# Kernel optimization log

Hardware: AMD Instinct MI355X
Metric: run time of the kernel (lower is better)

Reference implementation:

```python
import jax, jax.numpy as jnp
import numpy as np

C = 16        # C1 = C2 = Cout
LMAX = 2
# Sparse path set for Lmax=2, max_rank_other=1, allow_epsilon=False, k_policy='k0'.
# Enumeration order (L1 outer, L2 inner) matches the torch module's weight layout.
PATHS = [(0, 0), (0, 1), (0, 2), (1, 0), (1, 1), (2, 0)]  # Lout = L1 + L2, k_delta=0
# Fused einsums: contract channels a,b with per-path weight W[o,a,b];
# output tensor indices ordered as (free i's of A) then (free j's of B), per _einsum_for_path.
EQS = {
    (0, 0): 'na,nb,oab->no',
    (0, 1): 'na,nbi,oab->noi',
    (0, 2): 'na,nbij,oab->noij',
    (1, 0): 'nai,nb,oab->noi',
    (1, 1): 'nai,nbj,oab->noij',
    (2, 0): 'naij,nb,oab->noij',
}


def split_by_rank_o3(x, channels):
    """Split flat O(3)-graded features into {(s, L): block} with block shape (N, C, 3^L...)."""
    blocks = {}
    idx = 0
    n = x.shape[0]
    for s in (0, 1):
        for L in range(LMAX + 1):
            d = channels * 3 ** L
            blocks[(s, L)] = x[:, idx:idx + d].reshape((n, channels) + (3,) * L)
            idx += d
    return blocks


def _forward(x1, x2, weight):
    n = x1.shape[0]
    A = split_by_rank_o3(x1, C)
    B = split_by_rank_o3(x2, C)
    # assume_pseudo_zero & no epsilon: only s=0 blocks are used; s_out is always 0.
    out = {L: jnp.zeros((n, C) + (3,) * L, dtype=x1.dtype) for L in range(LMAX + 1)}
    w_idx = 0
    blk = C * C * C
    for (L1, L2) in PATHS:
        Wp = weight[w_idx:w_idx + blk].reshape(C, C, C)  # (Cout, C1, C2)
        w_idx += blk
        Lout = L1 + L2
        out[Lout] = out[Lout] + jnp.einsum(EQS[(L1, L2)], A[(0, L1)], B[(0, L2)], Wp)
    # merge_by_rank_o3: s=0 blocks (L=0..Lmax) then s=1 blocks (all zero here)
    parts = [out[L].reshape(n, -1) for L in range(LMAX + 1)]
    parts += [jnp.zeros((n, C * 3 ** L), dtype=x1.dtype) for L in range(LMAX + 1)]
    return jnp.concatenate(parts, axis=-1)  # (N, 2*C*13) = (N, 416)


def setup_inputs() -> dict:
    key = jax.random.key(0)
    k1, k2, k3 = jax.random.split(key, 3)
    N = 200000
    dim = 2 * C * (1 + 3 + 9)  # 416
    x1 = jax.random.normal(k1, (N, dim), dtype=jnp.float32)
    x2 = jax.random.normal(k2, (N, dim), dtype=jnp.float32)
    weight = jax.random.normal(k3, (len(PATHS) * C * C * C,), dtype=jnp.float32) * 0.02
    return {"x1": x1, "x2": x2, "weight": weight}


def reference(x1, x2, weight):
    return _forward(x1, x2, weight)
```

## Files before the change

kernel.cpp:

```cpp
#include <hip/hip_runtime.h>


constexpr int TILE_R  = 16;
constexpr int NTHR    = 256;
constexpr int WSTRIDE = 260;
constexpr int WSLICE  = 16 * WSTRIDE;
constexpr int RSTRIDE = 212;

__device__ __forceinline__ float dot16(const float* __restrict__ w, const float* a) {
    float s0 = 0.f, s1 = 0.f, s2 = 0.f, s3 = 0.f;
#pragma unroll
    for (int k = 0; k < 4; ++k) {
        float4 v = *(const float4*)(w + 4 * k);
        s0 = fmaf(v.x, a[4 * k + 0], s0);
        s1 = fmaf(v.y, a[4 * k + 1], s1);
        s2 = fmaf(v.z, a[4 * k + 2], s2);
        s3 = fmaf(v.w, a[4 * k + 3], s3);
    }
    return (s0 + s1) + (s2 + s3);
}

__device__ __forceinline__ void accum_t(const float* __restrict__ w,
                                        const float* a0, float* t) {
#pragma unroll
    for (int a = 0; a < 16; ++a) {
        float av = a0[a];
        const float* wr = w + 16 * a;
#pragma unroll
        for (int k = 0; k < 4; ++k) {
            float4 v = *(const float4*)(wr + 4 * k);
            t[4*k+0] = fmaf(v.x, av, t[4*k+0]);
            t[4*k+1] = fmaf(v.y, av, t[4*k+1]);
            t[4*k+2] = fmaf(v.z, av, t[4*k+2]);
            t[4*k+3] = fmaf(v.w, av, t[4*k+3]);
        }
    }
}

__device__ __forceinline__ void load_w2(const float* __restrict__ wgt, float* ws,
                                        int p0, int p1, int tid) {
#pragma unroll
    for (int s = tid; s < 2048; s += NTHR) {
        int m   = s >> 10;
        int rem = s & 1023;
        int oo  = rem >> 6;
        int off = (rem & 63) << 2;
        float4 v = *(const float4*)(wgt + (m ? p1 : p0) * 4096 + (rem << 2));
        *(float4*)&ws[m * WSLICE + oo * WSTRIDE + off] = v;
    }
}

__global__ __launch_bounds__(NTHR, 2)
void tp_kernel(const float* __restrict__ x1, const float* __restrict__ x2,
               const float* __restrict__ wgt, float* __restrict__ out, int N)
{
    __shared__ float Ws[2 * WSLICE];
    __shared__ float As[TILE_R * RSTRIDE];
    __shared__ float Bs[TILE_R * RSTRIDE];

    const int tid  = threadIdx.x;
    const int wave = tid >> 6;
    const int lane = tid & 63;
    const int o    = (wave << 2) + (lane >> 4);
    const int r    = lane & 15;
    const long long row0 = (long long)blockIdx.x * TILE_R;

    for (int idx = tid; idx < TILE_R * 52; idx += NTHR) {
        int rr = idx / 52, cc = idx - rr * 52;
        float4 va = make_float4(0.f, 0.f, 0.f, 0.f), vb = va;
        if (row0 + rr < N) {
            long long g = (row0 + rr) * 416 + cc * 4;
            va = *(const float4*)(x1 + g);
            vb = *(const float4*)(x2 + g);
        }
        *(float4*)&As[rr * RSTRIDE + cc * 4] = va;
        *(float4*)&Bs[rr * RSTRIDE + cc * 4] = vb;
    }
    load_w2(wgt, Ws, 0, 1, tid);
    __syncthreads();

    float a0[16], b0[16], b1[48];
#pragma unroll
    for (int k = 0; k < 4; ++k) {
        float4 v = *(const float4*)&As[r * RSTRIDE + 4 * k];
        a0[4*k+0] = v.x; a0[4*k+1] = v.y; a0[4*k+2] = v.z; a0[4*k+3] = v.w;
        float4 u = *(const float4*)&Bs[r * RSTRIDE + 4 * k];
        b0[4*k+0] = u.x; b0[4*k+1] = u.y; b0[4*k+2] = u.z; b0[4*k+3] = u.w;
    }
#pragma unroll
    for (int k = 0; k < 12; ++k) {
        float4 v = *(const float4*)&Bs[r * RSTRIDE + 16 + 4 * k];
        b1[4*k+0] = v.x; b1[4*k+1] = v.y; b1[4*k+2] = v.z; b1[4*k+3] = v.w;
    }

    float o0 = 0.f, o1[3] = {0.f, 0.f, 0.f};
    float o2[9] = {0.f,0.f,0.f,0.f,0.f,0.f,0.f,0.f,0.f};

    {
        const float* w0 = &Ws[o * WSTRIDE];
#pragma unroll
        for (int a = 0; a < 16; ++a)
            o0 = fmaf(a0[a], dot16(w0 + 16 * a, b0), o0);

        const float* w1 = &Ws[WSLICE + o * WSTRIDE];
        float t[16] = {0.f,0.f,0.f,0.f,0.f,0.f,0.f,0.f,0.f,0.f,0.f,0.f,0.f,0.f,0.f,0.f};
        accum_t(w1, a0, t);
#pragma unroll
        for (int b = 0; b < 16; ++b) {
            o1[0] = fmaf(t[b], b1[3*b+0], o1[0]);
            o1[1] = fmaf(t[b], b1[3*b+1], o1[1]);
            o1[2] = fmaf(t[b], b1[3*b+2], o1[2]);
        }
    }
    __syncthreads();
    load_w2(wgt, Ws, 2, 3, tid);
    __syncthreads();

    {
        const float* w2 = &Ws[o * WSTRIDE];
        float t[16] = {0.f,0.f,0.f,0.f,0.f,0.f,0.f,0.f,0.f,0.f,0.f,0.f,0.f,0.f,0.f,0.f};
        accum_t(w2, a0, t);
#pragma unroll
        for (int b = 0; b < 16; ++b) {
            const float* b2 = &Bs[r * RSTRIDE + 64 + 9 * b];
#pragma unroll
            for (int k = 0; k < 9; ++k) o2[k] = fmaf(t[b], b2[k], o2[k]);
        }

        const float* w3 = &Ws[WSLICE + o * WSTRIDE];
#pragma unroll
        for (int a = 0; a < 16; ++a) {
            float u = dot16(w3 + 16 * a, b0);
            const float* a1 = &As[r * RSTRIDE + 16 + 3 * a];
            o1[0] = fmaf(u, a1[0], o1[0]);
            o1[1] = fmaf(u, a1[1], o1[1]);
            o1[2] = fmaf(u, a1[2], o1[2]);
        }
    }
    __syncthreads();
    load_w2(wgt, Ws, 4, 5, tid);
    __syncthreads();

    {
        const float* w4 = &Ws[o * WSTRIDE];
#pragma unroll
        for (int a = 0; a < 16; ++a) {
            const float* wa = w4 + 16 * a;
            float v0 = 0.f, v1 = 0.f, v2 = 0.f;
#pragma unroll
            for (int k = 0; k < 4; ++k) {
                float4 w = *(const float4*)(wa + 4 * k);
                v0 = fmaf(w.x, b1[12*k+0], v0); v1 = fmaf(w.x, b1[12*k+ 1], v1); v2 = fmaf(w.x, b1[12*k+ 2], v2);
                v0 = fmaf(w.y, b1[12*k+3], v0); v1 = fmaf(w.y, b1[12*k+ 4], v1); v2 = fmaf(w.y, b1[12*k+ 5], v2);
                v0 = fmaf(w.z, b1[12*k+6], v0); v1 = fmaf(w.z, b1[12*k+ 7], v1); v2 = fmaf(w.z, b1[12*k+ 8], v2);
                v0 = fmaf(w.w, b1[12*k+9], v0); v1 = fmaf(w.w, b1[12*k+10], v1); v2 = fmaf(w.w, b1[12*k+11], v2);
            }
            const float* a1 = &As[r * RSTRIDE + 16 + 3 * a];
            float a10 = a1[0], a11 = a1[1], a12 = a1[2];
            o2[0] = fmaf(a10, v0, o2[0]); o2[1] = fmaf(a10, v1, o2[1]); o2[2] = fmaf(a10, v2, o2[2]);
            o2[3] = fmaf(a11, v0, o2[3]); o2[4] = fmaf(a11, v1, o2[4]); o2[5] = fmaf(a11, v2, o2[5]);
            o2[6] = fmaf(a12, v0, o2[6]); o2[7] = fmaf(a12, v1, o2[7]); o2[8] = fmaf(a12, v2, o2[8]);
        }

        const float* w5 = &Ws[WSLICE + o * WSTRIDE];
#pragma unroll
        for (int a = 0; a < 16; ++a) {
            float u = dot16(w5 + 16 * a, b0);
            const float* a2 = &As[r * RSTRIDE + 64 + 9 * a];
#pragma unroll
            for (int k = 0; k < 9; ++k) o2[k] = fmaf(u, a2[k], o2[k]);
        }
    }

    __syncthreads();
    {
        float* dst = &As[r * RSTRIDE];
        dst[o] = o0;
        dst[16 + 3*o + 0] = o1[0];
        dst[16 + 3*o + 1] = o1[1];
        dst[16 + 3*o + 2] = o1[2];
#pragma unroll
        for (int k = 0; k < 9; ++k) dst[64 + 9*o + k] = o2[k];
    }
    __syncthreads();
    for (int idx = tid; idx < TILE_R * 104; idx += NTHR) {
        int rr = idx / 104, cc = idx - rr * 104;
        if (row0 + rr < N) {
            float4 v = make_float4(0.f, 0.f, 0.f, 0.f);
            if (cc < 52) v = *(const float4*)&As[rr * RSTRIDE + (cc << 2)];
            *(float4*)&out[(row0 + rr) * 416 + (cc << 2)] = v;
        }
    }
}

extern "C" void kernel_launch(void* const* d_in, const int* in_sizes, int n_in,
                              void* d_out, int out_size, void* d_ws, size_t ws_size,
                              hipStream_t stream) {
    const float* x1  = (const float*)d_in[0];
    const float* x2  = (const float*)d_in[1];
    const float* wgt = (const float*)d_in[2];
    float* out = (float*)d_out;
    const int N = in_sizes[0] / 416;
    const int grid = (N + TILE_R - 1) / TILE_R;
    hipLaunchKernelGGL(tp_kernel, dim3(grid), dim3(NTHR), 0, stream, x1, x2, wgt, out, N);
}
```

Measured before the change: 988.4 us.

## Read weights from global via wave-uniform scalar loads and transpose activation tiles in LDS

The weight tiles are no longer staged in shared memory. Each wave now owns one output channel, selected with readfirstlane, so its weight reads are wave-uniform and can be served by scalar or cache loads straight from global memory. The block grows to 1024 threads and 64 rows, and the rank-1 and rank-2 activation blocks are stored transposed in LDS so each Cartesian component's 16 channels are contiguous for float4 reads. This removes the per-stage weight reload and its barriers, at the cost of larger blocks, lower occupancy flexibility and heavier register use.

```diff
diff --git a/kernel.cpp b/kernel.cpp
--- a/kernel.cpp
+++ b/kernel.cpp
@@ -1,11 +1,10 @@
 #include <hip/hip_runtime.h>
 
 
-constexpr int TILE_R  = 16;
-constexpr int NTHR    = 256;
-constexpr int WSTRIDE = 260;
-constexpr int WSLICE  = 16 * WSTRIDE;
-constexpr int RSTRIDE = 212;
+constexpr int NTHR   = 1024;
+constexpr int TILE_R = 64;
+constexpr int ASTR   = 228;
+constexpr int BSTR   = 212;
 
 __device__ __forceinline__ float dot16(const float* __restrict__ w, const float* a) {
     float s0 = 0.f, s1 = 0.f, s2 = 0.f, s3 = 0.f;
@@ -37,158 +36,153 @@
     }
 }
 
-__device__ __forceinline__ void load_w2(const float* __restrict__ wgt, float* ws,
-                                        int p0, int p1, int tid) {
-#pragma unroll
-    for (int s = tid; s < 2048; s += NTHR) {
-        int m   = s >> 10;
-        int rem = s & 1023;
-        int oo  = rem >> 6;
-        int off = (rem & 63) << 2;
-        float4 v = *(const float4*)(wgt + (m ? p1 : p0) * 4096 + (rem << 2));
-        *(float4*)&ws[m * WSLICE + oo * WSTRIDE + off] = v;
-    }
-}
-
-__global__ __launch_bounds__(NTHR, 2)
+__device__ __forceinline__ void ld16(const float* p, float* d) {
+#pragma unroll
+    for (int k = 0; k < 4; ++k) {
+        float4 v = *(const float4*)(p + 4 * k);
+        d[4*k+0] = v.x; d[4*k+1] = v.y; d[4*k+2] = v.z; d[4*k+3] = v.w;
+    }
+}
+
+__global__ __launch_bounds__(NTHR)
 void tp_kernel(const float* __restrict__ x1, const float* __restrict__ x2,
                const float* __restrict__ wgt, float* __restrict__ out, int N)
 {
-    __shared__ float Ws[2 * WSLICE];
-    __shared__ float As[TILE_R * RSTRIDE];
-    __shared__ float Bs[TILE_R * RSTRIDE];
-
-    const int tid  = threadIdx.x;
-    const int wave = tid >> 6;
-    const int lane = tid & 63;
-    const int o    = (wave << 2) + (lane >> 4);
-    const int r    = lane & 15;
+    __shared__ __align__(16) float As[TILE_R * ASTR];
+    __shared__ __align__(16) float Bs[TILE_R * BSTR];
+
+    const int tid = threadIdx.x;
     const long long row0 = (long long)blockIdx.x * TILE_R;
 
     for (int idx = tid; idx < TILE_R * 52; idx += NTHR) {
-        int rr = idx / 52, cc = idx - rr * 52;
+        int rr = idx / 52, c4 = idx - rr * 52;
         float4 va = make_float4(0.f, 0.f, 0.f, 0.f), vb = va;
         if (row0 + rr < N) {
-            long long g = (row0 + rr) * 416 + cc * 4;
+            long long g = (row0 + rr) * 416 + c4 * 4;
             va = *(const float4*)(x1 + g);
             vb = *(const float4*)(x2 + g);
         }
-        *(float4*)&As[rr * RSTRIDE + cc * 4] = va;
-        *(float4*)&Bs[rr * RSTRIDE + cc * 4] = vb;
-    }
-    load_w2(wgt, Ws, 0, 1, tid);
+        if (c4 < 4) {
+            *(float4*)&As[rr * ASTR + 4 * c4] = va;
+            *(float4*)&Bs[rr * BSTR + 4 * c4] = vb;
+        } else {
+            float fa[4] = {va.x, va.y, va.z, va.w};
+            float fb[4] = {vb.x, vb.y, vb.z, vb.w};
+#pragma unroll
+            for (int q = 0; q < 4; ++q) {
+                int c = 4 * c4 + q;
+                int da, db;
+                if (c < 64) {
+                    int n = c - 16;
+                    int a = (n * 21846) >> 16;
+                    int i = n - 3 * a;
+                    da = 16 + 4 * a + i;
+                    db = 16 + 16 * i + a;
+                } else {
+                    int n = c - 64;
+                    int a = (n * 7282) >> 16;
+                    int k = n - 9 * a;
+                    da = 80 + 16 * k + a;
+                    db = 64 + 16 * k + a;
+                }
+                As[rr * ASTR + da] = fa[q];
+                Bs[rr * BSTR + db] = fb[q];
+            }
+        }
+    }
     __syncthreads();
 
-    float a0[16], b0[16], b1[48];
-#pragma unroll
-    for (int k = 0; k < 4; ++k) {
-        float4 v = *(const float4*)&As[r * RSTRIDE + 4 * k];
-        a0[4*k+0] = v.x; a0[4*k+1] = v.y; a0[4*k+2] = v.z; a0[4*k+3] = v.w;
-        float4 u = *(const float4*)&Bs[r * RSTRIDE + 4 * k];
-        b0[4*k+0] = u.x; b0[4*k+1] = u.y; b0[4*k+2] = u.z; b0[4*k+3] = u.w;
-    }
-#pragma unroll
-    for (int k = 0; k < 12; ++k) {
-        float4 v = *(const float4*)&Bs[r * RSTRIDE + 16 + 4 * k];
-        b1[4*k+0] = v.x; b1[4*k+1] = v.y; b1[4*k+2] = v.z; b1[4*k+3] = v.w;
-    }
-
-    float o0 = 0.f, o1[3] = {0.f, 0.f, 0.f};
+    const int o = __builtin_amdgcn_readfirstlane((int)(threadIdx.x >> 6));
+    const int r = tid & 63;
+    const float* __restrict__ wp = wgt + o * 256;
+    const float* Ar = &As[r * ASTR];
+    const float* Br = &Bs[r * BSTR];
+
+    float a0[16], b0[16];
+    ld16(Ar, a0);
+    ld16(Br, b0);
+
+    float o0 = 0.f;
+    float o1[3] = {0.f, 0.f, 0.f};
     float o2[9] = {0.f,0.f,0.f,0.f,0.f,0.f,0.f,0.f,0.f};
 
+#pragma unroll
+    for (int a = 0; a < 16; ++a)
+        o0 = fmaf(a0[a], dot16(wp + 16 * a, b0), o0);
+
+    float t1[16], t2[16];
+#pragma unroll
+    for (int k = 0; k < 16; ++k) { t1[k] = 0.f; t2[k] = 0.f; }
+    accum_t(wp + 4096, a0, t1);
+    accum_t(wp + 8192, a0, t2);
+
+#pragma unroll
+    for (int j = 0; j < 3; ++j) {
+        float br[16];
+        ld16(Br + 16 + 16 * j, br);
+#pragma unroll
+        for (int b = 0; b < 16; ++b)
+            o1[j] = fmaf(t1[b], br[b], o1[j]);
+#pragma unroll
+        for (int a = 0; a < 16; ++a) {
+            float v = dot16(wp + 16384 + 16 * a, br);
+            float4 a1 = *(const float4*)(Ar + 16 + 4 * a);
+            o2[0 + j] = fmaf(a1.x, v, o2[0 + j]);
+            o2[3 + j] = fmaf(a1.y, v, o2[3 + j]);
+            o2[6 + j] = fmaf(a1.z, v, o2[6 + j]);
+        }
+    }
+
+#pragma unroll
+    for (int k = 0; k < 9; ++k) {
+        float br[16];
+        ld16(Br + 64 + 16 * k, br);
+#pragma unroll
+        for (int b = 0; b < 16; ++b)
+            o2[k] = fmaf(t2[b], br[b], o2[k]);
+    }
+
+#pragma unroll
+    for (int a = 0; a < 16; ++a) {
+        float u = dot16(wp + 12288 + 16 * a, b0);
+        float4 a1 = *(const float4*)(Ar + 16 + 4 * a);
+        o1[0] = fmaf(u, a1.x, o1[0]);
+        o1[1] = fmaf(u, a1.y, o1[1]);
+        o1[2] = fmaf(u, a1.z, o1[2]);
+    }
+
     {
-        const float* w0 = &Ws[o * WSTRIDE];
+        float u[16];
 #pragma unroll
         for (int a = 0; a < 16; ++a)
-            o0 = fmaf(a0[a], dot16(w0 + 16 * a, b0), o0);
-
-        const float* w1 = &Ws[WSLICE + o * WSTRIDE];
-        float t[16] = {0.f,0.f,0.f,0.f,0.f,0.f,0.f,0.f,0.f,0.f,0.f,0.f,0.f,0.f,0.f,0.f};
-        accum_t(w1, a0, t);
-#pragma unroll
-        for (int b = 0; b < 16; ++b) {
-            o1[0] = fmaf(t[b], b1[3*b+0], o1[0]);
-            o1[1] = fmaf(t[b], b1[3*b+1], o1[1]);
-            o1[2] = fmaf(t[b], b1[3*b+2], o1[2]);
-        }
-    }
-    __syncthreads();
-    load_w2(wgt, Ws, 2, 3, tid);
-    __syncthreads();
-
-    {
-        const float* w2 = &Ws[o * WSTRIDE];
-        float t[16] = {0.f,0.f,0.f,0.f,0.f,0.f,0.f,0.f,0.f,0.f,0.f,0.f,0.f,0.f,0.f,0.f};
-        accum_t(w2, a0, t);
-#pragma unroll
-        for (int b = 0; b < 16; ++b) {
-            const float* b2 = &Bs[r * RSTRIDE + 64 + 9 * b];
-#pragma unroll
-            for (int k = 0; k < 9; ++k) o2[k] = fmaf(t[b], b2[k], o2[k]);
-        }
-
-        const float* w3 = &Ws[WSLICE + o * WSTRIDE];
-#pragma unroll
-        for (int a = 0; a < 16; ++a) {
-            float u = dot16(w3 + 16 * a, b0);
-            const float* a1 = &As[r * RSTRIDE + 16 + 3 * a];
-            o1[0] = fmaf(u, a1[0], o1[0]);
-            o1[1] = fmaf(u, a1[1], o1[1]);
-            o1[2] = fmaf(u, a1[2], o1[2]);
-        }
-    }
-    __syncthreads();
-    load_w2(wgt, Ws, 4, 5, tid);
-    __syncthreads();
-
-    {
-        const float* w4 = &Ws[o * WSTRIDE];
-#pragma unroll
-        for (int a = 0; a < 16; ++a) {
-            const float* wa = w4 + 16 * a;
-            float v0 = 0.f, v1 = 0.f, v2 = 0.f;
-#pragma unroll
-            for (int k = 0; k < 4; ++k) {
-                float4 w = *(const float4*)(wa + 4 * k);
-                v0 = fmaf(w.x, b1[12*k+0], v0); v1 = fmaf(w.x, b1[12*k+ 1], v1); v2 = fmaf(w.x, b1[12*k+ 2], v2);
-                v0 = fmaf(w.y, b1[12*k+3], v0); v1 = fmaf(w.y, b1[12*k+ 4], v1); v2 = fmaf(w.y, b1[12*k+ 5], v2);
-                v0 = fmaf(w.z, b1[12*k+6], v0); v1 = fmaf(w.z, b1[12*k+ 7], v1); v2 = fmaf(w.z, b1[12*k+ 8], v2);
-                v0 = fmaf(w.w, b1[12*k+9], v0); v1 = fmaf(w.w, b1[12*k+10], v1); v2 = fmaf(w.w, b1[12*k+11], v2);
-            }
-            const float* a1 = &As[r * RSTRIDE + 16 + 3 * a];
-            float a10 = a1[0], a11 = a1[1], a12 = a1[2];
-            o2[0] = fmaf(a10, v0, o2[0]); o2[1] = fmaf(a10, v1, o2[1]); o2[2] = fmaf(a10, v2, o2[2]);
-            o2[3] = fmaf(a11, v0, o2[3]); o2[4] = fmaf(a11, v1, o2[4]); o2[5] = fmaf(a11, v2, o2[5]);
-            o2[6] = fmaf(a12, v0, o2[6]); o2[7] = fmaf(a12, v1, o2[7]); o2[8] = fmaf(a12, v2, o2[8]);
-        }
-
-        const float* w5 = &Ws[WSLICE + o * WSTRIDE];
-#pragma unroll
-        for (int a = 0; a < 16; ++a) {
-            float u = dot16(w5 + 16 * a, b0);
-            const float* a2 = &As[r * RSTRIDE + 64 + 9 * a];
-#pragma unroll
-            for (int k = 0; k < 9; ++k) o2[k] = fmaf(u, a2[k], o2[k]);
+            u[a] = dot16(wp + 20480 + 16 * a, b0);
+#pragma unroll
+        for (int k = 0; k < 9; ++k) {
+            float ar[16];
+            ld16(Ar + 80 + 16 * k, ar);
+#pragma unroll
+            for (int a = 0; a < 16; ++a)
+                o2[k] = fmaf(u[a], ar[a], o2[k]);
         }
     }
 
     __syncthreads();
     {
-        float* dst = &As[r * RSTRIDE];
+        float* dst = &As[r * ASTR];
         dst[o] = o0;
-        dst[16 + 3*o + 0] = o1[0];
-        dst[16 + 3*o + 1] = o1[1];
-        dst[16 + 3*o + 2] = o1[2];
-#pragma unroll
-        for (int k = 0; k < 9; ++k) dst[64 + 9*o + k] = o2[k];
+        dst[16 + 3 * o + 0] = o1[0];
+        dst[16 + 3 * o + 1] = o1[1];
+        dst[16 + 3 * o + 2] = o1[2];
+#pragma unroll
+        for (int k = 0; k < 9; ++k) dst[64 + 9 * o + k] = o2[k];
     }
     __syncthreads();
     for (int idx = tid; idx < TILE_R * 104; idx += NTHR) {
-        int rr = idx / 104, cc = idx - rr * 104;
+        int rr = idx / 104, c4 = idx - rr * 104;
         if (row0 + rr < N) {
             float4 v = make_float4(0.f, 0.f, 0.f, 0.f);
-            if (cc < 52) v = *(const float4*)&As[rr * RSTRIDE + (cc << 2)];
-            *(float4*)&out[(row0 + rr) * 416 + (cc << 2)] = v;
+            if (c4 < 52) v = *(const float4*)&As[rr * ASTR + 4 * c4];
+            *(float4*)&out[(row0 + rr) * 416 + 4 * c4] = v;
         }
     }
 }
```

Result: slower. 1.690 ms (+70.9%).
